# Kernel optimization log

Hardware: AMD Instinct MI355X
Metric: run time of the kernel (lower is better)

Reference implementation:

```python
import jax, jax.numpy as jnp
import numpy as np

B, C, H, W = 4, 256, 64, 64
CQK = C // 2


def setup_inputs() -> dict:
    key = jax.random.key(0)
    ks = jax.random.split(key, 8)
    s = 0.05
    return {
        "x": jax.random.normal(ks[0], (B, C, H, W), dtype=jnp.float32),
        "wq": jax.random.normal(ks[1], (CQK, C), dtype=jnp.float32) * s,
        "bq": jax.random.normal(ks[2], (CQK,), dtype=jnp.float32) * s,
        "wk": jax.random.normal(ks[3], (CQK, C), dtype=jnp.float32) * s,
        "bk": jax.random.normal(ks[4], (CQK,), dtype=jnp.float32) * s,
        "wv": jax.random.normal(ks[5], (C, C), dtype=jnp.float32) * s,
        "bv": jax.random.normal(ks[6], (C,), dtype=jnp.float32) * s,
        "gamma": jax.random.normal(ks[7], (1,), dtype=jnp.float32),
    }


def reference(x, wq, bq, wk, bk, wv, bv, gamma):
    b, c, h, w = x.shape
    n = h * w
    xf = x.reshape(b, c, n)  # [B,C,N]
    # 1x1 convs == per-pixel linear projections
    q = jnp.einsum("oc,bcn->bon", wq, xf) + bq[:, None]  # [B,C/2,N]
    k = jnp.einsum("oc,bcn->bon", wk, xf) + bk[:, None]  # [B,C/2,N]
    v = jnp.einsum("oc,bcn->bon", wv, xf) + bv[:, None]  # [B,C,N]
    # attention[b,m,n'] = softmax_n'( sum_d q[b,d,m] * k[b,d,n'] )
    scores = jnp.einsum("bdm,bdn->bmn", q, k)  # [B,N,N]
    attn = jax.nn.softmax(scores, axis=2)
    # out_feat[b,c,j] = sum_i v[b,c,i] * attn[b,i,j]  (matmul(value, attention))
    af = jnp.einsum("bci,bij->bcj", v, attn)  # [B,C,N]
    out = gamma[0] * af.reshape(b, c, h, w) + x
    return out
```

## Files before the change

kernel.cpp:

```cpp
#include <hip/hip_runtime.h>
#include <hip/hip_bf16.h>


typedef _Float16 f16;
typedef _Float16 f16x4v __attribute__((ext_vector_type(4)));
typedef _Float16 f16x8v __attribute__((ext_vector_type(8)));
typedef float f32x4v __attribute__((ext_vector_type(4)));
typedef unsigned short u16;
typedef unsigned short u16x4v __attribute__((ext_vector_type(4)));
typedef unsigned short u16x8v __attribute__((ext_vector_type(8)));
typedef short s16x8v __attribute__((ext_vector_type(8)));

static __device__ __forceinline__ f32x4v mfma16(f16x8v a, f16x8v b, f32x4v c) {
  return __builtin_amdgcn_mfma_f32_16x16x32_f16(a, b, c, 0, 0, 0);
}
static __device__ __forceinline__ f32x4v mfma_bf(s16x8v a, s16x8v b, f32x4v c) {
  return __builtin_amdgcn_mfma_f32_16x16x32_bf16(a, b, c, 0, 0, 0);
}
static __device__ __forceinline__ u16 f2bf(float f) {
  union { __hip_bfloat16 h; u16 u; } cv;
  cv.h = __float2bfloat16(f);
  return cv.u;
}

#define AS1q __attribute__((address_space(1)))
#define AS3q __attribute__((address_space(3)))
static __device__ __forceinline__ void gl_lds16(const void* g, void* l) {
  __builtin_amdgcn_global_load_lds((const AS1q unsigned int*)g,
                                   (AS3q unsigned int*)l, 16, 0, 0);
}

__global__ void k_wcvt(const float* __restrict__ wq, const float* __restrict__ bq,
                       const float* __restrict__ wk, const float* __restrict__ bk,
                       const float* __restrict__ wv, const float* __restrict__ bv,
                       f16* __restrict__ wh, float* __restrict__ bcat) {
  int o = blockIdx.x;
  int c = threadIdx.x;
  const float* wrow; float bias;
  if (o < 128)      { wrow = wq + (size_t)o * 256;         bias = bq[o]; }
  else if (o < 256) { wrow = wk + (size_t)(o - 128) * 256; bias = bk[o - 128]; }
  else              { wrow = wv + (size_t)(o - 256) * 256; bias = bv[o - 256]; }
  wh[(size_t)o * 256 + c] = (f16)wrow[c];
  if (c == 0) bcat[o] = bias;
}

__global__ void k_xsplit(const float* __restrict__ x, f16* __restrict__ xh) {
  __shared__ float t[64][65];
  int b = blockIdx.z, c0 = blockIdx.y * 64, n0 = blockIdx.x * 64;
  int tx = threadIdx.x & 63, ty = threadIdx.x >> 6;
  const float* xb = x + ((size_t)b * 256 + c0) * 4096 + n0;
#pragma unroll
  for (int r = ty; r < 64; r += 4) t[r][tx] = xb[(size_t)r * 4096 + tx];
  __syncthreads();
  f16* dh = xh + ((size_t)b * 4096 + n0) * 256 + c0;
#pragma unroll
  for (int r = ty; r < 64; r += 4)
    dh[(size_t)r * 256 + tx] = (f16)t[tx][r];
}

__global__ void __launch_bounds__(256, 2)
k_proj(const f16* __restrict__ xh, const f16* __restrict__ wh,
       const float* __restrict__ bcat, f16* __restrict__ qk, f16* __restrict__ vv) {
  extern __shared__ char smem[];
  int b = blockIdx.z, m0 = blockIdx.y * 64, n0 = blockIdx.x * 64;
  int tid = threadIdx.x, l = tid & 63, w = tid >> 6;
  int col = l & 15, quad = l >> 4;
  const f16* Ag = xh + ((size_t)b * 4096 + m0) * 256;
  const f16* Wg = wh + (size_t)n0 * 256;
  int rloc = l >> 5;
  int l5 = l & 31;
#pragma unroll
  for (int p = 0; p < 8; p++) {
    int ci = w * 8 + p;
    int r = ci * 2 + rloc;
    int g = l5 ^ (r & 31);
    gl_lds16(Ag + (size_t)r * 256 + g * 8, smem + ci * 1024);
    gl_lds16(Wg + (size_t)r * 256 + g * 8, smem + 32768 + ci * 1024);
  }
  __syncthreads();
  const char* sA = smem;
  const char* sW = smem + 32768;
  f32x4v acc[4] = {};
  int ar = w * 16 + col;
#pragma unroll
  for (int ks = 0; ks < 8; ks++) {
    int G = ks * 4 + quad;
    f16x8v a = *(const f16x8v*)(sA + ar * 512 + ((G ^ (ar & 31)) * 16));
#pragma unroll
    for (int nt = 0; nt < 4; nt++) {
      int wr = nt * 16 + col;
      f16x8v bb = *(const f16x8v*)(sW + wr * 512 + ((G ^ (wr & 31)) * 16));
      acc[nt] = mfma16(a, bb, acc[nt]);
    }
  }
  bool isqk = (n0 < 256);
#pragma unroll
  for (int nt = 0; nt < 4; nt++) {
    int o = n0 + nt * 16 + col;
    float bias = bcat[o];
    if (isqk) {
#pragma unroll
      for (int rg = 0; rg < 4; rg++) {
        int i = m0 + w * 16 + quad * 4 + rg;
        qk[((size_t)b * 4096 + i) * 256 + o] = (f16)(acc[nt][rg] + bias);
      }
    } else {
      int i = m0 + w * 16 + quad * 4;
      f16x4v pv;
#pragma unroll
      for (int rg = 0; rg < 4; rg++) pv[rg] = (f16)(acc[nt][rg] + bias);
      *(f16x4v*)&vv[((size_t)b * 256 + (o - 256)) * 4096 + i] = pv;
    }
  }
}

__global__ void __launch_bounds__(256, 2)
k_pmake(const f16* __restrict__ qk, u16* __restrict__ P, float* __restrict__ partial) {
  __shared__ char smem[49152];
  f16* sQ = (f16*)smem;
  f16* sK = (f16*)(smem + 32768);
  u16* sPT = (u16*)smem;
  int b = blockIdx.z, i0 = blockIdx.y * 128, j0 = blockIdx.x * 64;
  int tid = threadIdx.x, l = tid & 63, w = tid >> 6;
  int col = l & 15, q = l >> 4;
  const f16* qb = qk + (size_t)b * 4096 * 256;
#pragma unroll
  for (int p = 0; p < 8; p++) {
    int ci = w * 8 + p;
    int r = ci * 4 + (l >> 4);
    int cb = (l & 15) ^ (r & 15);
    gl_lds16(qb + (size_t)(i0 + r) * 256 + cb * 8, smem + ci * 1024);
  }
#pragma unroll
  for (int p = 0; p < 4; p++) {
    int ci = w * 4 + p;
    int r = ci * 4 + (l >> 4);
    int cb = (l & 15) ^ (r & 15);
    gl_lds16(qb + (size_t)(j0 + r) * 256 + 128 + cb * 8, smem + 32768 + ci * 1024);
  }
  __syncthreads();
  f32x4v acc[2][4] = {};
#pragma unroll
  for (int ks = 0; ks < 4; ks++) {
    int phys = (ks * 4 + q) ^ col;
    f16x8v a[2], bb[4];
#pragma unroll
    for (int mt = 0; mt < 2; mt++)
      a[mt] = *(const f16x8v*)&sQ[(w * 32 + mt * 16 + col) * 128 + phys * 8];
#pragma unroll
    for (int nt = 0; nt < 4; nt++)
      bb[nt] = *(const f16x8v*)&sK[(nt * 16 + col) * 128 + phys * 8];
#pragma unroll
    for (int mt = 0; mt < 2; mt++)
#pragma unroll
      for (int nt = 0; nt < 4; nt++)
        acc[mt][nt] = mfma16(a[mt], bb[nt], acc[mt][nt]);
  }
  float pe[2][4][4];
#pragma unroll
  for (int mt = 0; mt < 2; mt++)
#pragma unroll
    for (int nt = 0; nt < 4; nt++)
#pragma unroll
      for (int rg = 0; rg < 4; rg++)
        pe[mt][nt][rg] = __expf(acc[mt][nt][rg]);
  __syncthreads();
#pragma unroll
  for (int mt = 0; mt < 2; mt++) {
    int ib = w * 32 + mt * 16 + q * 4;
#pragma unroll
    for (int nt = 0; nt < 4; nt++) {
      u16x4v pw;
#pragma unroll
      for (int rg = 0; rg < 4; rg++) pw[rg] = f2bf(pe[mt][nt][rg]);
      *(u16x4v*)&sPT[(nt * 16 + col) * 132 + ib] = pw;
    }
  }
#pragma unroll
  for (int mt = 0; mt < 2; mt++) {
    f32x4v cs;
#pragma unroll
    for (int rg = 0; rg < 4; rg++) {
      float t = pe[mt][0][rg] + pe[mt][1][rg] + pe[mt][2][rg] + pe[mt][3][rg];
#pragma unroll
      for (int d = 1; d < 16; d <<= 1) t += __shfl_xor(t, d, 64);
      cs[rg] = t;
    }
    if (col == 0) {
      size_t base = ((size_t)b * 64 + blockIdx.x) * 4096 + i0 + w * 32 + mt * 16 + q * 4;
      *(f32x4v*)&partial[base] = cs;
    }
  }
  __syncthreads();
  u16* Pb = P + ((size_t)b * 4096 + j0) * 4096 + i0;
#pragma unroll
  for (int p = 0; p < 4; p++) {
    int slot = p * 256 + tid;
    int jr = slot >> 4, c16 = slot & 15;
    *(u16x8v*)&Pb[(size_t)jr * 4096 + c16 * 8] =
        *(const u16x8v*)&sPT[jr * 132 + c16 * 8];
  }
}

__global__ void k_rsum(const float* __restrict__ partial, float* __restrict__ rowsum) {
  int b = blockIdx.y;
  int i = blockIdx.x * 256 + threadIdx.x;
  const float* p = partial + (size_t)b * 64 * 4096 + i;
  float s = 0.f;
#pragma unroll 8
  for (int jb = 0; jb < 64; jb++) s += p[(size_t)jb * 4096];
  rowsum[(size_t)b * 4096 + i] = s;
}

__global__ void k_scalev(u16* __restrict__ vvb, const float* __restrict__ rowsum) {
  size_t idx = ((size_t)blockIdx.x * 256 + threadIdx.x) * 8;
  int i = (int)(idx & 4095);
  int b = (int)(idx >> 20);
  f16x8v v = *(f16x8v*)&vvb[idx];
  const float* rs = rowsum + ((size_t)b << 12) + i;
  u16x8v o;
#pragma unroll
  for (int t = 0; t < 8; t++) o[t] = f2bf((float)v[t] * (1.0f / rs[t]));
  *(u16x8v*)&vvb[idx] = o;
}

__global__ void __launch_bounds__(512, 2)
k_av(const u16* __restrict__ vv, const u16* __restrict__ P,
     const float* __restrict__ x, const float* __restrict__ gamma,
     float* __restrict__ out) {
  extern __shared__ char smem[];
  int b = blockIdx.z, c0 = blockIdx.x * 128, j0 = blockIdx.y * 128;
  int tid = threadIdx.x, l = tid & 63, w = tid >> 6;
  int col = l & 15, q = l >> 4;
  int cw = w >> 2, jw = w & 3;
  const u16* Ab = vv + ((size_t)b * 256 + c0) * 4096;
  const u16* Bb = P + ((size_t)b * 4096 + j0) * 4096;
  int rloc = l >> 3;
  int gsw = l & 7;
  f32x4v acc[4][2] = {};
#pragma unroll
  for (int p = 0; p < 4; p++) {
    int ci = w * 4 + p;
    int rr = (ci & 15) * 8 + rloc;
    int g = gsw ^ (rr & 7);
    const u16* src = (ci < 16 ? Ab : Bb) + (size_t)rr * 4096 + g * 8;
    gl_lds16(src, smem + ci * 1024);
  }
  for (int it = 0; it < 64; it++) {
    __syncthreads();
    if (it < 63) {
      int k0 = (it + 1) * 64;
      char* nb = smem + ((it + 1) & 1) * 32768;
#pragma unroll
      for (int p = 0; p < 4; p++) {
        int ci = w * 4 + p;
        int rr = (ci & 15) * 8 + rloc;
        int g = gsw ^ (rr & 7);
        const u16* src = (ci < 16 ? Ab : Bb) + (size_t)rr * 4096 + k0 + g * 8;
        gl_lds16(src, nb + ci * 1024);
      }
    }
    const char* cur = smem + (it & 1) * 32768;
#pragma unroll
    for (int ks = 0; ks < 2; ks++) {
      int G = ks * 4 + q;
      s16x8v a[4], bb[2];
#pragma unroll
      for (int mt = 0; mt < 4; mt++) {
        int ar = cw * 64 + mt * 16 + col;
        a[mt] = *(const s16x8v*)(cur + ar * 128 + ((G ^ (ar & 7)) * 16));
      }
#pragma unroll
      for (int nt = 0; nt < 2; nt++) {
        int jr = jw * 32 + nt * 16 + col;
        bb[nt] = *(const s16x8v*)(cur + 16384 + jr * 128 + ((G ^ (jr & 7)) * 16));
      }
#pragma unroll
      for (int mt = 0; mt < 4; mt++)
#pragma unroll
        for (int nt = 0; nt < 2; nt++)
          acc[mt][nt] = mfma_bf(a[mt], bb[nt], acc[mt][nt]);
    }
  }
  float g = gamma[0];
#pragma unroll
  for (int mt = 0; mt < 4; mt++)
#pragma unroll
    for (int nt = 0; nt < 2; nt++) {
      int c = c0 + cw * 64 + mt * 16 + q * 4;
      int j = j0 + jw * 32 + nt * 16 + col;
#pragma unroll
      for (int rg = 0; rg < 4; rg++) {
        size_t off = ((size_t)b * 256 + c + rg) * 4096 + j;
        out[off] = g * acc[mt][nt][rg] + x[off];
      }
    }
}

extern "C" void kernel_launch(void* const* d_in, const int* in_sizes, int n_in,
                              void* d_out, int out_size, void* d_ws, size_t ws_size,
                              hipStream_t stream) {
  (void)in_sizes; (void)n_in; (void)out_size; (void)ws_size;
  const float* x  = (const float*)d_in[0];
  const float* wq = (const float*)d_in[1];
  const float* bq = (const float*)d_in[2];
  const float* wk = (const float*)d_in[3];
  const float* bk = (const float*)d_in[4];
  const float* wv = (const float*)d_in[5];
  const float* bv = (const float*)d_in[6];
  const float* gm = (const float*)d_in[7];
  float* out = (float*)d_out;

  char* ws = (char*)d_ws;
  const size_t P_BYTES = (size_t)4 * 4096 * 4096 * 2;
  u16*  Pt = (u16*)(ws);
  f16*  xh = (f16*)(ws);
  char* tail = ws + P_BYTES;
  f16*  qk = (f16*)(tail);
  u16*  vv = (u16*)(tail + 8388608);
  f16*  wh = (f16*)(tail + 16777216);
  float* bcat    = (float*)(tail + 17039360);
  float* rowsum  = (float*)(tail + 17041408);
  float* partial = (float*)(tail + 17106944);

  hipLaunchKernelGGL(k_wcvt, dim3(512), dim3(256), 0, stream, wq, bq, wk, bk, wv, bv, wh, bcat);
  hipLaunchKernelGGL(k_xsplit, dim3(64, 4, 4), dim3(256), 0, stream, x, xh);
  hipLaunchKernelGGL(k_proj, dim3(8, 64, 4), dim3(256), 65536, stream, xh, wh, bcat, qk, (f16*)vv);
  hipLaunchKernelGGL(k_pmake, dim3(64, 32, 4), dim3(256), 0, stream, qk, Pt, partial);
  hipLaunchKernelGGL(k_rsum, dim3(16, 4), dim3(256), 0, stream, partial, rowsum);
  hipLaunchKernelGGL(k_scalev, dim3(2048), dim3(256), 0, stream, vv, rowsum);
  hipLaunchKernelGGL(k_av, dim3(2, 32, 4), dim3(512), 65536, stream, vv, Pt, x, gm, out);
}
```

Baseline: 202.9 us.

## Recompute attention scores inside AV kernel instead of materializing P matrix

The 4x4096x4096 bf16 probability matrix is no longer written to and read back from global memory. A first pass (k_sums) computes only the per-row exp sums, and the AV kernel recomputes QK^T tiles on the fly, exponentiates them into LDS and multiplies by the pre-scaled V. The Q weights are pre-scaled by log2(e) so exp2f can replace expf. The cost is computing QK^T twice and a new AV kernel with one block per 64 columns spanning all 256 channels, which gives only 256 blocks at occupancy 1 and adds two barriers per iteration.

New measurement: 214.8 us. 1.06x slower.

```diff
diff --git a/kernel.cpp b/kernel.cpp
--- a/kernel.cpp
+++ b/kernel.cpp
@@ -30,18 +30,20 @@
                                    (AS3q unsigned int*)l, 16, 0, 0);
 }
 
+#define LOG2E 1.4426950408889634f
+
 __global__ void k_wcvt(const float* __restrict__ wq, const float* __restrict__ bq,
                        const float* __restrict__ wk, const float* __restrict__ bk,
                        const float* __restrict__ wv, const float* __restrict__ bv,
                        f16* __restrict__ wh, float* __restrict__ bcat) {
   int o = blockIdx.x;
   int c = threadIdx.x;
-  const float* wrow; float bias;
-  if (o < 128)      { wrow = wq + (size_t)o * 256;         bias = bq[o]; }
+  const float* wrow; float bias; float scale = 1.0f;
+  if (o < 128)      { wrow = wq + (size_t)o * 256;         bias = bq[o]; scale = LOG2E; }
   else if (o < 256) { wrow = wk + (size_t)(o - 128) * 256; bias = bk[o - 128]; }
   else              { wrow = wv + (size_t)(o - 256) * 256; bias = bv[o - 256]; }
-  wh[(size_t)o * 256 + c] = (f16)wrow[c];
-  if (c == 0) bcat[o] = bias;
+  wh[(size_t)o * 256 + c] = (f16)(wrow[c] * scale);
+  if (c == 0) bcat[o] = bias * scale;
 }
 
 __global__ void k_xsplit(const float* __restrict__ x, f16* __restrict__ xh) {
@@ -115,100 +117,68 @@
 }
 
 __global__ void __launch_bounds__(256, 2)
-k_pmake(const f16* __restrict__ qk, u16* __restrict__ P, float* __restrict__ partial) {
-  __shared__ char smem[49152];
-  f16* sQ = (f16*)smem;
-  f16* sK = (f16*)(smem + 32768);
-  u16* sPT = (u16*)smem;
-  int b = blockIdx.z, i0 = blockIdx.y * 128, j0 = blockIdx.x * 64;
+k_sums(const f16* __restrict__ qk, float* __restrict__ partial) {
+  extern __shared__ char smem[];
+  int b = blockIdx.z, i0 = blockIdx.y * 128, j0 = blockIdx.x * 128;
   int tid = threadIdx.x, l = tid & 63, w = tid >> 6;
-  int col = l & 15, q = l >> 4;
-  const f16* qb = qk + (size_t)b * 4096 * 256;
+  int col = l & 15, quad = l >> 4;
+  const char* qb = (const char*)(qk + (size_t)b * 4096 * 256);
 #pragma unroll
   for (int p = 0; p < 8; p++) {
     int ci = w * 8 + p;
     int r = ci * 4 + (l >> 4);
-    int cb = (l & 15) ^ (r & 15);
-    gl_lds16(qb + (size_t)(i0 + r) * 256 + cb * 8, smem + ci * 1024);
-  }
-#pragma unroll
-  for (int p = 0; p < 4; p++) {
-    int ci = w * 4 + p;
-    int r = ci * 4 + (l >> 4);
-    int cb = (l & 15) ^ (r & 15);
-    gl_lds16(qb + (size_t)(j0 + r) * 256 + 128 + cb * 8, smem + 32768 + ci * 1024);
+    int g = (l & 15) ^ (r & 15);
+    gl_lds16(qb + (size_t)(i0 + r) * 512 + g * 16, smem + ci * 1024);
+    gl_lds16(qb + (size_t)(j0 + r) * 512 + 256 + g * 16, smem + 32768 + ci * 1024);
   }
   __syncthreads();
-  f32x4v acc[2][4] = {};
+  const char* sQ = smem;
+  const char* sK = smem + 32768;
+  f32x4v acc[2][8] = {};
 #pragma unroll
   for (int ks = 0; ks < 4; ks++) {
-    int phys = (ks * 4 + q) ^ col;
-    f16x8v a[2], bb[4];
-#pragma unroll
-    for (int mt = 0; mt < 2; mt++)
-      a[mt] = *(const f16x8v*)&sQ[(w * 32 + mt * 16 + col) * 128 + phys * 8];
-#pragma unroll
-    for (int nt = 0; nt < 4; nt++)
-      bb[nt] = *(const f16x8v*)&sK[(nt * 16 + col) * 128 + phys * 8];
-#pragma unroll
-    for (int mt = 0; mt < 2; mt++)
-#pragma unroll
-      for (int nt = 0; nt < 4; nt++)
-        acc[mt][nt] = mfma16(a[mt], bb[nt], acc[mt][nt]);
-  }
-  float pe[2][4][4];
-#pragma unroll
-  for (int mt = 0; mt < 2; mt++)
-#pragma unroll
-    for (int nt = 0; nt < 4; nt++)
-#pragma unroll
-      for (int rg = 0; rg < 4; rg++)
-        pe[mt][nt][rg] = __expf(acc[mt][nt][rg]);
-  __syncthreads();
-#pragma unroll
-  for (int mt = 0; mt < 2; mt++) {
-    int ib = w * 32 + mt * 16 + q * 4;
-#pragma unroll
-    for (int nt = 0; nt < 4; nt++) {
-      u16x4v pw;
-#pragma unroll
-      for (int rg = 0; rg < 4; rg++) pw[rg] = f2bf(pe[mt][nt][rg]);
-      *(u16x4v*)&sPT[(nt * 16 + col) * 132 + ib] = pw;
-    }
-  }
-#pragma unroll
-  for (int mt = 0; mt < 2; mt++) {
+    int G = ks * 4 + quad;
+    f16x8v a[2];
+#pragma unroll
+    for (int it = 0; it < 2; it++) {
+      int ar = (w * 2 + it) * 16 + col;
+      a[it] = *(const f16x8v*)(sQ + ar * 256 + ((G ^ (ar & 15)) * 16));
+    }
+#pragma unroll
+    for (int jt = 0; jt < 8; jt++) {
+      int jr = jt * 16 + col;
+      f16x8v kb = *(const f16x8v*)(sK + jr * 256 + ((G ^ (jr & 15)) * 16));
+#pragma unroll
+      for (int it = 0; it < 2; it++)
+        acc[it][jt] = mfma16(a[it], kb, acc[it][jt]);
+    }
+  }
+#pragma unroll
+  for (int it = 0; it < 2; it++) {
     f32x4v cs;
 #pragma unroll
     for (int rg = 0; rg < 4; rg++) {
-      float t = pe[mt][0][rg] + pe[mt][1][rg] + pe[mt][2][rg] + pe[mt][3][rg];
+      float t = 0.f;
+#pragma unroll
+      for (int jt = 0; jt < 8; jt++) t += exp2f(acc[it][jt][rg]);
 #pragma unroll
       for (int d = 1; d < 16; d <<= 1) t += __shfl_xor(t, d, 64);
       cs[rg] = t;
     }
     if (col == 0) {
-      size_t base = ((size_t)b * 64 + blockIdx.x) * 4096 + i0 + w * 32 + mt * 16 + q * 4;
+      size_t base = ((size_t)b * 32 + blockIdx.x) * 4096 + i0 + (w * 2 + it) * 16 + quad * 4;
       *(f32x4v*)&partial[base] = cs;
     }
-  }
-  __syncthreads();
-  u16* Pb = P + ((size_t)b * 4096 + j0) * 4096 + i0;
-#pragma unroll
-  for (int p = 0; p < 4; p++) {
-    int slot = p * 256 + tid;
-    int jr = slot >> 4, c16 = slot & 15;
-    *(u16x8v*)&Pb[(size_t)jr * 4096 + c16 * 8] =
-        *(const u16x8v*)&sPT[jr * 132 + c16 * 8];
   }
 }
 
 __global__ void k_rsum(const float* __restrict__ partial, float* __restrict__ rowsum) {
   int b = blockIdx.y;
   int i = blockIdx.x * 256 + threadIdx.x;
-  const float* p = partial + (size_t)b * 64 * 4096 + i;
+  const float* p = partial + (size_t)b * 32 * 4096 + i;
   float s = 0.f;
 #pragma unroll 8
-  for (int jb = 0; jb < 64; jb++) s += p[(size_t)jb * 4096];
+  for (int jb = 0; jb < 32; jb++) s += p[(size_t)jb * 4096];
   rowsum[(size_t)b * 4096 + i] = s;
 }
 
@@ -224,71 +194,99 @@
   *(u16x8v*)&vvb[idx] = o;
 }
 
-__global__ void __launch_bounds__(512, 2)
-k_av(const u16* __restrict__ vv, const u16* __restrict__ P,
-     const float* __restrict__ x, const float* __restrict__ gamma,
-     float* __restrict__ out) {
+__global__ void __launch_bounds__(512, 1)
+k_av2(const f16* __restrict__ qk, const u16* __restrict__ vv,
+      const float* __restrict__ x, const float* __restrict__ gamma,
+      float* __restrict__ out) {
   extern __shared__ char smem[];
-  int b = blockIdx.z, c0 = blockIdx.x * 128, j0 = blockIdx.y * 128;
+  char* sQ = smem;
+  char* sV = smem + 16384;
+  u16*  sP = (u16*)(smem + 49152);
+  int b = blockIdx.y, j0 = blockIdx.x * 64;
   int tid = threadIdx.x, l = tid & 63, w = tid >> 6;
-  int col = l & 15, q = l >> 4;
-  int cw = w >> 2, jw = w & 3;
-  const u16* Ab = vv + ((size_t)b * 256 + c0) * 4096;
-  const u16* Bb = P + ((size_t)b * 4096 + j0) * 4096;
-  int rloc = l >> 3;
-  int gsw = l & 7;
-  f32x4v acc[4][2] = {};
-#pragma unroll
-  for (int p = 0; p < 4; p++) {
-    int ci = w * 4 + p;
-    int rr = (ci & 15) * 8 + rloc;
-    int g = gsw ^ (rr & 7);
-    const u16* src = (ci < 16 ? Ab : Bb) + (size_t)rr * 4096 + g * 8;
-    gl_lds16(src, smem + ci * 1024);
-  }
+  int col = l & 15, quad = l >> 4;
+  const char* qb = (const char*)(qk + (size_t)b * 4096 * 256);
+  const char* Vb = (const char*)(vv + (size_t)b * 256 * 4096);
+  int itile = w >> 1;
+  int jsel = (w & 1) * 2;
+  f16x8v kfr[2][4];
+#pragma unroll
+  for (int e = 0; e < 2; e++)
+#pragma unroll
+    for (int ks = 0; ks < 4; ks++)
+      kfr[e][ks] = *(const f16x8v*)(qb + (size_t)(j0 + (jsel + e) * 16 + col) * 512 +
+                                    256 + (ks * 4 + quad) * 16);
+#pragma unroll
+  for (int p = 0; p < 2; p++) {
+    int ci = w * 2 + p;
+    int r = ci * 4 + (l >> 4);
+    int g = (l & 15) ^ (r & 15);
+    gl_lds16(qb + (size_t)r * 512 + g * 16, sQ + ci * 1024);
+  }
+  f32x4v acc[2][4] = {};
   for (int it = 0; it < 64; it++) {
     __syncthreads();
-    if (it < 63) {
-      int k0 = (it + 1) * 64;
-      char* nb = smem + ((it + 1) & 1) * 32768;
+    {
+      int i0b = it * 128;
 #pragma unroll
       for (int p = 0; p < 4; p++) {
         int ci = w * 4 + p;
-        int rr = (ci & 15) * 8 + rloc;
-        int g = gsw ^ (rr & 7);
-        const u16* src = (ci < 16 ? Ab : Bb) + (size_t)rr * 4096 + k0 + g * 8;
-        gl_lds16(src, nb + ci * 1024);
-      }
-    }
-    const char* cur = smem + (it & 1) * 32768;
+        int r = ci * 8 + (l >> 3);
+        int g = (l & 7) ^ (r & 7);
+        gl_lds16(Vb + (size_t)r * 8192 + i0b + g * 16, sV + ci * 1024);
+      }
+    }
+    f32x4v s[2] = {};
+#pragma unroll
+    for (int ks = 0; ks < 4; ks++) {
+      int ar = itile * 16 + col;
+      f16x8v a = *(const f16x8v*)(sQ + ar * 256 + (((ks * 4 + quad) ^ (ar & 15)) * 16));
+#pragma unroll
+      for (int e = 0; e < 2; e++) s[e] = mfma16(a, kfr[e][ks], s[e]);
+    }
+#pragma unroll
+    for (int e = 0; e < 2; e++) {
+      u16x4v pw;
+#pragma unroll
+      for (int rg = 0; rg < 4; rg++) pw[rg] = f2bf(exp2f(s[e][rg]));
+      *(u16x4v*)&sP[((jsel + e) * 16 + col) * 72 + itile * 16 + quad * 4] = pw;
+    }
+    __syncthreads();
+    if (it < 63) {
+      int i0n = (it + 1) * 64;
+#pragma unroll
+      for (int p = 0; p < 2; p++) {
+        int ci = w * 2 + p;
+        int r = ci * 4 + (l >> 4);
+        int g = (l & 15) ^ (r & 15);
+        gl_lds16(qb + (size_t)(i0n + r) * 512 + g * 16, sQ + ci * 1024);
+      }
+    }
 #pragma unroll
     for (int ks = 0; ks < 2; ks++) {
-      int G = ks * 4 + q;
-      s16x8v a[4], bb[2];
-#pragma unroll
-      for (int mt = 0; mt < 4; mt++) {
-        int ar = cw * 64 + mt * 16 + col;
-        a[mt] = *(const s16x8v*)(cur + ar * 128 + ((G ^ (ar & 7)) * 16));
-      }
-#pragma unroll
-      for (int nt = 0; nt < 2; nt++) {
-        int jr = jw * 32 + nt * 16 + col;
-        bb[nt] = *(const s16x8v*)(cur + 16384 + jr * 128 + ((G ^ (jr & 7)) * 16));
-      }
-#pragma unroll
-      for (int mt = 0; mt < 4; mt++)
-#pragma unroll
-        for (int nt = 0; nt < 2; nt++)
-          acc[mt][nt] = mfma_bf(a[mt], bb[nt], acc[mt][nt]);
+      s16x8v a[2];
+#pragma unroll
+      for (int mt = 0; mt < 2; mt++) {
+        int cr = (w * 2 + mt) * 16 + col;
+        a[mt] = *(const s16x8v*)(sV + cr * 128 + (((ks * 4 + quad) ^ (cr & 7)) * 16));
+      }
+#pragma unroll
+      for (int nt = 0; nt < 4; nt++) {
+        s16x8v pb = *(const s16x8v*)((const char*)sP + (nt * 16 + col) * 144 +
+                                     (ks * 4 + quad) * 16);
+#pragma unroll
+        for (int mt = 0; mt < 2; mt++)
+          acc[mt][nt] = mfma_bf(a[mt], pb, acc[mt][nt]);
+      }
     }
   }
   float g = gamma[0];
 #pragma unroll
-  for (int mt = 0; mt < 4; mt++)
-#pragma unroll
-    for (int nt = 0; nt < 2; nt++) {
-      int c = c0 + cw * 64 + mt * 16 + q * 4;
-      int j = j0 + jw * 32 + nt * 16 + col;
+  for (int mt = 0; mt < 2; mt++)
+#pragma unroll
+    for (int nt = 0; nt < 4; nt++) {
+      int c = (w * 2 + mt) * 16 + quad * 4;
+      int j = j0 + nt * 16 + col;
 #pragma unroll
       for (int rg = 0; rg < 4; rg++) {
         size_t off = ((size_t)b * 256 + c + rg) * 4096 + j;
@@ -312,22 +310,19 @@
   float* out = (float*)d_out;
 
   char* ws = (char*)d_ws;
-  const size_t P_BYTES = (size_t)4 * 4096 * 4096 * 2;
-  u16*  Pt = (u16*)(ws);
   f16*  xh = (f16*)(ws);
-  char* tail = ws + P_BYTES;
-  f16*  qk = (f16*)(tail);
-  u16*  vv = (u16*)(tail + 8388608);
-  f16*  wh = (f16*)(tail + 16777216);
-  float* bcat    = (float*)(tail + 17039360);
-  float* rowsum  = (float*)(tail + 17041408);
-  float* partial = (float*)(tail + 17106944);
+  f16*  qk = (f16*)(ws + 8388608);
+  u16*  vv = (u16*)(ws + 16777216);
+  f16*  wh = (f16*)(ws + 25165824);
+  float* bcat    = (float*)(ws + 25427968);
+  float* rowsum  = (float*)(ws + 25430016);
+  float* partial = (float*)(ws + 25495552);
 
   hipLaunchKernelGGL(k_wcvt, dim3(512), dim3(256), 0, stream, wq, bq, wk, bk, wv, bv, wh, bcat);
   hipLaunchKernelGGL(k_xsplit, dim3(64, 4, 4), dim3(256), 0, stream, x, xh);
   hipLaunchKernelGGL(k_proj, dim3(8, 64, 4), dim3(256), 65536, stream, xh, wh, bcat, qk, (f16*)vv);
-  hipLaunchKernelGGL(k_pmake, dim3(64, 32, 4), dim3(256), 0, stream, qk, Pt, partial);
+  hipLaunchKernelGGL(k_sums, dim3(32, 32, 4), dim3(256), 65536, stream, qk, partial);
   hipLaunchKernelGGL(k_rsum, dim3(16, 4), dim3(256), 0, stream, partial, rowsum);
   hipLaunchKernelGGL(k_scalev, dim3(2048), dim3(256), 0, stream, vv, rowsum);
-  hipLaunchKernelGGL(k_av, dim3(2, 32, 4), dim3(512), 65536, stream, vv, Pt, x, gm, out);
-}
+  hipLaunchKernelGGL(k_av2, dim3(64, 4), dim3(512), 58368, stream, qk, vv, x, gm, out);
+}
```
